# Performance work log

Measured on AMD Instinct MI355X. Metric: run time of the kernel, lower is better.

## Reference

```python
import jax, jax.numpy as jnp
import numpy as np

N = 50000      # nodes
E = 600000     # edges
F_IN = 9       # atom features
H = 128        # hidden dim
G = 2048       # graphs in batch
EPS = 1e-5     # batchnorm eps


def setup_inputs() -> dict:
    key = jax.random.key(0)
    ks = jax.random.split(key, 24)

    def lin(k, i, o):
        return (jax.random.normal(k, (i, o), jnp.float32) / np.sqrt(i).astype(np.float32))

    x = jax.random.normal(ks[0], (N, F_IN), jnp.float32)
    edge_index = jax.random.randint(ks[1], (2, E), 0, N, dtype=jnp.int32)
    # deterministic sorted graph assignment: every graph non-empty (~24 nodes each)
    batch = ((jnp.arange(N, dtype=jnp.int32) * G) // N).astype(jnp.int32)

    return {
        "x": x, "edge_index": edge_index, "batch": batch,
        "W0": lin(ks[2], F_IN, H), "b0": jnp.zeros((H,), jnp.float32),
        "g0": jnp.ones((H,), jnp.float32), "be0": jnp.zeros((H,), jnp.float32),
        "W1": lin(ks[3], H, H), "b1": jnp.zeros((H,), jnp.float32),
        "g1": jnp.ones((H,), jnp.float32), "be1": jnp.zeros((H,), jnp.float32),
        "W2": lin(ks[4], H, H), "b2": jnp.zeros((H,), jnp.float32),
        "g2": jnp.ones((H,), jnp.float32), "be2": jnp.zeros((H,), jnp.float32),
        "fc1_w": lin(ks[5], 2 * H, H), "fc1_b": jnp.zeros((H,), jnp.float32),
        "fc2_w": lin(ks[6], H, H // 2), "fc2_b": jnp.zeros((H // 2,), jnp.float32),
        "out_w": lin(ks[7], H // 2, 5), "out_b": jnp.zeros((5,), jnp.float32),
    }


def _gcn_conv(x, src, dst, W, b):
    # PyG GCNConv: add self-loops, symmetric deg^-1/2 normalization.
    h = x @ W                                   # [N, H_out]
    deg = jax.ops.segment_sum(jnp.ones((E,), h.dtype), dst, num_segments=N) + 1.0
    dis = jax.lax.rsqrt(deg)                    # deg^-1/2 incl. self-loop
    coef = dis[src] * dis[dst]                  # [E]
    agg = jax.ops.segment_sum(h[src] * coef[:, None], dst, num_segments=N)
    agg = agg + h * (dis * dis)[:, None]        # self-loop messages
    return agg + b


def _bn_relu(x, g, b):
    m = jnp.mean(x, axis=0)
    v = jnp.mean(jnp.square(x - m), axis=0)     # biased variance (torch BN)
    return jax.nn.relu((x - m) * jax.lax.rsqrt(v + EPS) * g + b)


def reference(x, edge_index, batch,
              W0, b0, g0, be0, W1, b1, g1, be1, W2, b2, g2, be2,
              fc1_w, fc1_b, fc2_w, fc2_b, out_w, out_b):
    src, dst = edge_index[0], edge_index[1]

    h = _bn_relu(_gcn_conv(x, src, dst, W0, b0), g0, be0)
    h = _bn_relu(_gcn_conv(h, src, dst, W1, b1), g1, be1)
    h = _bn_relu(_gcn_conv(h, src, dst, W2, b2), g2, be2)

    counts = jax.ops.segment_sum(jnp.ones((N,), h.dtype), batch, num_segments=G)
    x_mean = jax.ops.segment_sum(h, batch, num_segments=G) / jnp.maximum(counts, 1.0)[:, None]
    x_max = jax.ops.segment_max(h, batch, num_segments=G)

    z = jnp.concatenate([x_mean, x_max], axis=1)        # [G, 2H]
    z = jax.nn.relu(z @ fc1_w + fc1_b)
    z = jax.nn.relu(z @ fc2_w + fc2_b)
    return z @ out_w + out_b                            # [G, 5]
```

## Files before the change

kernel.cpp:

```cpp
#include <hip/hip_runtime.h>
#include <hip/hip_bf16.h>

#define N_NODES 50000
#define N_EDGES 600000
#define F_INX 9
#define HD 128
#define G_GRAPHS 2048
#define BN_EPS 1e-5f

#define SCAN_CHUNK 1024
#define SCAN_BLOCKS ((N_NODES + SCAN_CHUNK - 1) / SCAN_CHUNK)
#define BN_SLICES 16
#define BN_LAYER_F (BN_SLICES * 256)

#define NB_LIN0 3125
#define NB_WCONV 16
#define NB_ZCNT 196
#define NB_ZBN 48
#define NB_PRE (NB_LIN0 + NB_WCONV + NB_ZCNT + NB_ZBN)

typedef __bf16 bf16x8 __attribute__((ext_vector_type(8)));
typedef float f32x4 __attribute__((ext_vector_type(4)));

__device__ inline unsigned short f2bf(float f) {
    union { float f; unsigned u; } v;
    v.f = f;
    unsigned r = v.u + 0x7fff + ((v.u >> 16) & 1);
    return (unsigned short)(r >> 16);
}
__device__ inline float asf(unsigned u) {
    union { unsigned u; float f; } v;
    v.u = u;
    return v.f;
}
__device__ inline unsigned packbf(float a, float b) {
    return (unsigned)f2bf(a) | ((unsigned)f2bf(b) << 16);
}

__global__ __launch_bounds__(256) void k_preamble(
        const float* __restrict__ x, const float* __restrict__ W0,
        const float* __restrict__ W1, const float* __restrict__ W2,
        int* __restrict__ cnt, float* __restrict__ bnacc,
        unsigned short* __restrict__ wf1, unsigned short* __restrict__ wf2,
        unsigned short* __restrict__ hout) {
    int b = blockIdx.x, t = threadIdx.x;
    if (b < NB_LIN0) {
        __shared__ float rows[16][F_INX];
        int node0 = b * 16;
        for (int i = t; i < 16 * F_INX; i += 256)
            rows[i / F_INX][i % F_INX] = x[(size_t)node0 * F_INX + i];
        __syncthreads();
        int half = t >> 7, c = t & 127;
        float acc[8];
#pragma unroll
        for (int n = 0; n < 8; ++n) acc[n] = 0.0f;
#pragma unroll
        for (int k = 0; k < F_INX; ++k) {
            float w = W0[k * HD + c];
#pragma unroll
            for (int n = 0; n < 8; ++n) acc[n] += rows[half * 8 + n][k] * w;
        }
#pragma unroll
        for (int n = 0; n < 8; ++n)
            hout[(size_t)(node0 + half * 8 + n) * HD + c] = f2bf(acc[n]);
    } else if (b < NB_LIN0 + NB_WCONV) {
        int bw = b - NB_LIN0;
        const float* W = (bw < 8) ? W1 : W2;
        unsigned short* Wf = (bw < 8) ? wf1 : wf2;
        int triple = (bw & 7) * 256 + t;
        int kb = triple >> 9;
        int rest = triple & 511;
        int nt = rest >> 6;
        int l = rest & 63;
        int quad = l >> 4, lc = l & 15;
#pragma unroll
        for (int j = 0; j < 8; ++j)
            Wf[(size_t)triple * 8 + j] =
                f2bf(W[(size_t)(kb * 32 + quad * 8 + j) * HD + nt * 16 + lc]);
    } else if (b < NB_LIN0 + NB_WCONV + NB_ZCNT) {
        int idx = (b - NB_LIN0 - NB_WCONV) * 256 + t;
        if (idx < N_NODES) cnt[idx] = 0;
    } else {
        int idx = (b - NB_LIN0 - NB_WCONV - NB_ZCNT) * 256 + t;
        if (idx < 3 * BN_LAYER_F) bnacc[idx] = 0.0f;
    }
}

__global__ void k_count(const int* __restrict__ dst, int* __restrict__ cnt) {
    int e = blockIdx.x * blockDim.x + threadIdx.x;
    if (e < N_EDGES) atomicAdd(&cnt[dst[e]], 1);
}

__global__ void k_scanA(const int* __restrict__ cnt, int* __restrict__ blocksum) {
    __shared__ int red[256];
    int b = blockIdx.x, t = threadIdx.x;
    int idx = b * SCAN_CHUNK + t * 4;
    int s = 0;
    if (idx + 3 < N_NODES) {
        int4 v = *(const int4*)(cnt + idx);
        s = v.x + v.y + v.z + v.w;
    }
    red[t] = s;
    __syncthreads();
    for (int off = 128; off > 0; off >>= 1) {
        if (t < off) red[t] += red[t + off];
        __syncthreads();
    }
    if (t == 0) blocksum[b] = red[0];
}

__global__ void k_scanC(const int* __restrict__ cnt, const int* __restrict__ blocksum,
                        int* __restrict__ rowptr, int* __restrict__ cursor,
                        float* __restrict__ dis) {
    __shared__ int pre[256];
    __shared__ int myoff_s;
    int b = blockIdx.x, t = threadIdx.x;
    if (t < 64) {
        int v = (t < SCAN_BLOCKS) ? blocksum[t] : 0;
        int incl = v;
        for (int off = 1; off < 64; off <<= 1) {
            int u = __shfl_up(incl, off, 64);
            if (t >= off) incl += u;
        }
        if (t == b) myoff_s = incl - v;
    }
    int idx = b * SCAN_CHUNK + t * 4;
    int4 v = make_int4(0, 0, 0, 0);
    bool valid = (idx + 3 < N_NODES);
    if (valid) v = *(const int4*)(cnt + idx);
    int s = v.x + v.y + v.z + v.w;
    pre[t] = s;
    __syncthreads();
    for (int off = 1; off < 256; off <<= 1) {
        int u = (t >= off) ? pre[t - off] : 0;
        __syncthreads();
        pre[t] += u;
        __syncthreads();
    }
    if (valid) {
        int base = myoff_s + pre[t] - s;
        int4 rp;
        rp.x = base;
        rp.y = base + v.x;
        rp.z = rp.y + v.y;
        rp.w = rp.z + v.z;
        *(int4*)(rowptr + idx) = rp;
        *(int4*)(cursor + idx) = rp;
        float4 dv = make_float4(rsqrtf((float)v.x + 1.0f), rsqrtf((float)v.y + 1.0f),
                                rsqrtf((float)v.z + 1.0f), rsqrtf((float)v.w + 1.0f));
        *(float4*)(dis + idx) = dv;
    }
}

__global__ void k_scatter(const int* __restrict__ src, const int* __restrict__ dst,
                          const float* __restrict__ dis, int* __restrict__ cursor,
                          unsigned* __restrict__ ebuf) {
    int e = blockIdx.x * blockDim.x + threadIdx.x;
    if (e >= N_EDGES) return;
    int s = src[e], d = dst[e];
    int pos = atomicAdd(&cursor[d], 1);
    float coef = dis[s] * dis[d];
    ebuf[pos] = (unsigned)(s & 0xffff) | ((unsigned)f2bf(coef) << 16);
}

#define LIN_ROWS 64
#define ATS 136

__global__ __launch_bounds__(256, 4) void k_linear_mfma(
        const unsigned* __restrict__ agg32, const unsigned short* __restrict__ Wf,
        const float* __restrict__ bnp, const float* __restrict__ gam,
        const float* __restrict__ bet, unsigned short* __restrict__ hout) {
    __shared__ __align__(16) unsigned short At[LIN_ROWS][ATS];
    __shared__ float sc_s[HD], sh_s[HD];
    int node0 = blockIdx.x * LIN_ROWS;
    int t = threadIdx.x;

    if (t < HD) {
        float s = 0.0f, q = 0.0f;
#pragma unroll
        for (int i = 0; i < BN_SLICES; ++i) {
            s += bnp[i * 256 + t];
            q += bnp[i * 256 + 128 + t];
        }
        const float inv_n = 1.0f / (float)N_NODES;
        float m = s * inv_n;
        float v = q * inv_n - m * m;
        float sc = gam[t] * rsqrtf(v + BN_EPS);
        sc_s[t] = sc;
        sh_s[t] = bet[t] - m * sc;
    }
    __syncthreads();

    for (int i = t; i < LIN_ROWS * 16; i += 256) {
        int r = i >> 4;
        int c8 = (i & 15) * 8;
        int node = node0 + r;
        uint4 u = make_uint4(0, 0, 0, 0);
        if (node < N_NODES) u = *(const uint4*)(agg32 + (size_t)node * 64 + c8 / 2);
        unsigned uu[4] = {u.x, u.y, u.z, u.w};
        unsigned short o[8];
#pragma unroll
        for (int j = 0; j < 4; ++j) {
            float e = asf(uu[j] << 16);
            float od = asf(uu[j] & 0xffff0000u);
            int ce = c8 + 2 * j, co = ce + 1;
            o[2 * j] = f2bf(fmaxf(0.f, e * sc_s[ce] + sh_s[ce]));
            o[2 * j + 1] = f2bf(fmaxf(0.f, od * sc_s[co] + sh_s[co]));
        }
        *(ushort4*)&At[r][c8] = *(ushort4*)&o[0];
        *(ushort4*)&At[r][c8 + 4] = *(ushort4*)&o[4];
    }
    __syncthreads();

    int w = t >> 6, l = t & 63;
    int quad = l >> 4, lc = l & 15;
    int arow = w * 16 + lc;
    int koff = quad * 8;

    f32x4 acc[8];
#pragma unroll
    for (int nt = 0; nt < 8; ++nt) acc[nt] = (f32x4){0.f, 0.f, 0.f, 0.f};

#pragma unroll
    for (int kb = 0; kb < 4; ++kb) {
        bf16x8 af = *(const bf16x8*)&At[arow][kb * 32 + koff];
#pragma unroll
        for (int nt = 0; nt < 8; ++nt) {
            bf16x8 bfg = *(const bf16x8*)&Wf[(size_t)(((kb * 8) + nt) * 64 + l) * 8];
            acc[nt] = __builtin_amdgcn_mfma_f32_16x16x32_bf16(af, bfg, acc[nt], 0, 0, 0);
        }
    }

    int node_base = node0 + w * 16 + quad * 4;
#pragma unroll
    for (int nt = 0; nt < 8; ++nt) {
#pragma unroll
        for (int r = 0; r < 4; ++r) {
            int node = node_base + r;
            if (node < N_NODES)
                hout[(size_t)node * HD + nt * 16 + lc] = f2bf(acc[nt][r]);
        }
    }
}

__global__ __launch_bounds__(256, 8) void k_gather(
        const int* __restrict__ rowptr, const int* __restrict__ cnt,
        const unsigned* __restrict__ ebuf, const unsigned short* __restrict__ h,
        const float* __restrict__ dis, unsigned* __restrict__ agg32,
        float* __restrict__ bnp) {
    __shared__ float redS[4][256];
    __shared__ float redQ[4][256];
    int wv = threadIdx.x >> 6;
    int lane = threadIdx.x & 63;
    int node = __builtin_amdgcn_readfirstlane(blockIdx.x * 4 + wv);
    const unsigned* h32 = (const unsigned*)h;

    int start = rowptr[node];
    int deg = cnt[node];
    float d = dis[node];
    unsigned sv = h32[(size_t)node * 64 + lane];
    float dd = d * d;
    float acc0 = asf(sv << 16) * dd;
    float acc1 = asf(sv & 0xffff0000u) * dd;

    int e = start, end = start + deg;
    for (; e + 4 <= end; e += 4) {
        unsigned r0 = ebuf[e], r1 = ebuf[e + 1], r2 = ebuf[e + 2], r3 = ebuf[e + 3];
        unsigned hv0 = h32[(size_t)(r0 & 0xffffu) * 64 + lane];
        unsigned hv1 = h32[(size_t)(r1 & 0xffffu) * 64 + lane];
        unsigned hv2 = h32[(size_t)(r2 & 0xffffu) * 64 + lane];
        unsigned hv3 = h32[(size_t)(r3 & 0xffffu) * 64 + lane];
        float c0 = asf(r0 & 0xffff0000u), c1 = asf(r1 & 0xffff0000u);
        float c2 = asf(r2 & 0xffff0000u), c3 = asf(r3 & 0xffff0000u);
        acc0 += asf(hv0 << 16) * c0;
        acc1 += asf(hv0 & 0xffff0000u) * c0;
        acc0 += asf(hv1 << 16) * c1;
        acc1 += asf(hv1 & 0xffff0000u) * c1;
        acc0 += asf(hv2 << 16) * c2;
        acc1 += asf(hv2 & 0xffff0000u) * c2;
        acc0 += asf(hv3 << 16) * c3;
        acc1 += asf(hv3 & 0xffff0000u) * c3;
    }
    for (; e < end; ++e) {
        unsigned r = ebuf[e];
        unsigned hv = h32[(size_t)(r & 0xffffu) * 64 + lane];
        float cf = asf(r & 0xffff0000u);
        acc0 += asf(hv << 16) * cf;
        acc1 += asf(hv & 0xffff0000u) * cf;
    }

    agg32[(size_t)node * 64 + lane] = packbf(acc0, acc1);

    redS[wv][2 * lane] = acc0;
    redS[wv][2 * lane + 1] = acc1;
    redQ[wv][2 * lane] = acc0 * acc0;
    redQ[wv][2 * lane + 1] = acc1 * acc1;
    __syncthreads();
    int t = threadIdx.x;
    int ch = t & 127;
    int which = t >> 7;
    float val;
    if (which == 0)
        val = redS[0][ch] + redS[1][ch] + redS[2][ch] + redS[3][ch];
    else
        val = redQ[0][ch] + redQ[1][ch] + redQ[2][ch] + redQ[3][ch];
    int slice = blockIdx.x & (BN_SLICES - 1);
    atomicAdd(&bnp[slice * 256 + which * 128 + ch], val);
}

__global__ void k_head(const unsigned short* __restrict__ agg16,
                       const float* __restrict__ bnp, const float* __restrict__ gam,
                       const float* __restrict__ bet, const float* __restrict__ fc1_w,
                       const float* __restrict__ fc1_b, const float* __restrict__ fc2_w,
                       const float* __restrict__ fc2_b, const float* __restrict__ out_w,
                       const float* __restrict__ out_b, float* __restrict__ out) {
    __shared__ float z[2 * HD];
    __shared__ float z1[HD];
    __shared__ float z2[64];
    int g = blockIdx.x, c = threadIdx.x;
    float s = 0.0f, q = 0.0f;
#pragma unroll
    for (int i = 0; i < BN_SLICES; ++i) {
        s += bnp[i * 256 + c];
        q += bnp[i * 256 + 128 + c];
    }
    const float inv_n = 1.0f / (float)N_NODES;
    float m = s * inv_n;
    float v = q * inv_n - m * m;
    float sc = gam[c] * rsqrtf(v + BN_EPS);
    float sh = bet[c] - m * sc;
    int start = (g * N_NODES + G_GRAPHS - 1) / G_GRAPHS;
    int end = ((g + 1) * N_NODES + G_GRAPHS - 1) / G_GRAPHS;
    float sm = 0.0f, mx = 0.0f;
    for (int n = start; n < end; ++n) {
        float raw = asf((unsigned)agg16[(size_t)n * HD + c] << 16);
        float val = fmaxf(0.0f, raw * sc + sh);
        sm += val;
        mx = fmaxf(mx, val);
    }
    z[c] = sm / (float)(end - start);
    z[HD + c] = mx;
    __syncthreads();
    float a1 = fc1_b[c];
#pragma unroll 8
    for (int k = 0; k < 2 * HD; ++k) a1 += z[k] * fc1_w[k * HD + c];
    z1[c] = fmaxf(a1, 0.0f);
    __syncthreads();
    if (c < 64) {
        float a2 = fc2_b[c];
#pragma unroll 8
        for (int k = 0; k < HD; ++k) a2 += z1[k] * fc2_w[k * 64 + c];
        z2[c] = fmaxf(a2, 0.0f);
    }
    __syncthreads();
    if (c < 5) {
        float a3 = out_b[c];
#pragma unroll
        for (int k = 0; k < 64; ++k) a3 += z2[k] * out_w[k * 5 + c];
        out[(size_t)g * 5 + c] = a3;
    }
}

extern "C" void kernel_launch(void* const* d_in, const int* in_sizes, int n_in,
                              void* d_out, int out_size, void* d_ws, size_t ws_size,
                              hipStream_t stream) {
    const float* x = (const float*)d_in[0];
    const int* edge_index = (const int*)d_in[1];
    const float* W0 = (const float*)d_in[3];
    const float* g0 = (const float*)d_in[5];
    const float* be0 = (const float*)d_in[6];
    const float* W1 = (const float*)d_in[7];
    const float* g1 = (const float*)d_in[9];
    const float* be1 = (const float*)d_in[10];
    const float* W2 = (const float*)d_in[11];
    const float* g2 = (const float*)d_in[13];
    const float* be2 = (const float*)d_in[14];
    const float* fc1_w = (const float*)d_in[15];
    const float* fc1_b = (const float*)d_in[16];
    const float* fc2_w = (const float*)d_in[17];
    const float* fc2_b = (const float*)d_in[18];
    const float* out_w = (const float*)d_in[19];
    const float* out_b = (const float*)d_in[20];
    float* out = (float*)d_out;

    const int* src = edge_index;
    const int* dst = edge_index + N_EDGES;

    char* ws = (char*)d_ws;
    size_t off = 0;
    auto alloc = [&](size_t bytes) {
        char* p = ws + off;
        off += (bytes + 255) & ~(size_t)255;
        return p;
    };
    int* cnt = (int*)alloc(N_NODES * 4);
    int* rowptr = (int*)alloc(N_NODES * 4);
    int* cursor = (int*)alloc(N_NODES * 4);
    float* dis = (float*)alloc(N_NODES * 4);
    int* blocksum = (int*)alloc(SCAN_BLOCKS * 4);
    unsigned* ebuf = (unsigned*)alloc((size_t)N_EDGES * 4);
    unsigned short* hbuf = (unsigned short*)alloc((size_t)N_NODES * HD * 2);
    unsigned* aggbuf = (unsigned*)alloc((size_t)N_NODES * 64 * 4);
    float* bnacc = (float*)alloc((size_t)3 * BN_LAYER_F * 4);
    unsigned short* wf1 = (unsigned short*)alloc(HD * HD * 2);
    unsigned short* wf2 = (unsigned short*)alloc(HD * HD * 2);
    (void)ws_size;

    float* bnp0 = bnacc + 0 * BN_LAYER_F;
    float* bnp1 = bnacc + 1 * BN_LAYER_F;
    float* bnp2 = bnacc + 2 * BN_LAYER_F;

    k_preamble<<<NB_PRE, 256, 0, stream>>>(x, W0, W1, W2, cnt, bnacc, wf1, wf2, hbuf);
    k_count<<<(N_EDGES + 255) / 256, 256, 0, stream>>>(dst, cnt);
    k_scanA<<<SCAN_BLOCKS, 256, 0, stream>>>(cnt, blocksum);
    k_scanC<<<SCAN_BLOCKS, 256, 0, stream>>>(cnt, blocksum, rowptr, cursor, dis);
    k_scatter<<<(N_EDGES + 255) / 256, 256, 0, stream>>>(src, dst, dis, cursor, ebuf);

    const int LIN_GRID = (N_NODES + LIN_ROWS - 1) / LIN_ROWS;
    const int GATHER_GRID = N_NODES / 4;

    k_gather<<<GATHER_GRID, 256, 0, stream>>>(rowptr, cnt, ebuf, hbuf, dis, aggbuf, bnp0);
    k_linear_mfma<<<LIN_GRID, 256, 0, stream>>>(aggbuf, wf1, bnp0, g0, be0, hbuf);
    k_gather<<<GATHER_GRID, 256, 0, stream>>>(rowptr, cnt, ebuf, hbuf, dis, aggbuf, bnp1);
    k_linear_mfma<<<LIN_GRID, 256, 0, stream>>>(aggbuf, wf2, bnp1, g1, be1, hbuf);
    k_gather<<<GATHER_GRID, 256, 0, stream>>>(rowptr, cnt, ebuf, hbuf, dis, aggbuf, bnp2);

    k_head<<<G_GRAPHS, HD, 0, stream>>>((const unsigned short*)aggbuf, bnp2, g2, be2,
                                        fc1_w, fc1_b, fc2_w, fc2_b, out_w, out_b, out);
}
```

Baseline: 330.4 us.

## Coarsen gather to four nodes per wave with 16-wide batched edge loads

Each wave in the gather kernel now processes four destination nodes in sequence instead of one, and the grid shrinks to match. The edge loop issues 16 predicated edge-record loads and 16 neighbour-row loads before accumulating, so more memory requests are in flight per wave. Per-wave BN partial sums are accumulated across the four nodes, which cuts shared-memory reductions and global atomics by four. The cost is fewer total waves, so load balancing and latency hiding across waves suffer, and padded lanes issue wasted loads of row 0 because average degree is around 12.

```diff
diff --git a/kernel.cpp b/kernel.cpp
--- a/kernel.cpp
+++ b/kernel.cpp
@@ -243,6 +243,8 @@
     }
 }
 
+#define GN 16
+
 __global__ __launch_bounds__(256, 8) void k_gather(
         const int* __restrict__ rowptr, const int* __restrict__ cnt,
         const unsigned* __restrict__ ebuf, const unsigned short* __restrict__ h,
@@ -252,49 +254,50 @@
     __shared__ float redQ[4][256];
     int wv = threadIdx.x >> 6;
     int lane = threadIdx.x & 63;
-    int node = __builtin_amdgcn_readfirstlane(blockIdx.x * 4 + wv);
     const unsigned* h32 = (const unsigned*)h;
-
-    int start = rowptr[node];
-    int deg = cnt[node];
-    float d = dis[node];
-    unsigned sv = h32[(size_t)node * 64 + lane];
-    float dd = d * d;
-    float acc0 = asf(sv << 16) * dd;
-    float acc1 = asf(sv & 0xffff0000u) * dd;
-
-    int e = start, end = start + deg;
-    for (; e + 4 <= end; e += 4) {
-        unsigned r0 = ebuf[e], r1 = ebuf[e + 1], r2 = ebuf[e + 2], r3 = ebuf[e + 3];
-        unsigned hv0 = h32[(size_t)(r0 & 0xffffu) * 64 + lane];
-        unsigned hv1 = h32[(size_t)(r1 & 0xffffu) * 64 + lane];
-        unsigned hv2 = h32[(size_t)(r2 & 0xffffu) * 64 + lane];
-        unsigned hv3 = h32[(size_t)(r3 & 0xffffu) * 64 + lane];
-        float c0 = asf(r0 & 0xffff0000u), c1 = asf(r1 & 0xffff0000u);
-        float c2 = asf(r2 & 0xffff0000u), c3 = asf(r3 & 0xffff0000u);
-        acc0 += asf(hv0 << 16) * c0;
-        acc1 += asf(hv0 & 0xffff0000u) * c0;
-        acc0 += asf(hv1 << 16) * c1;
-        acc1 += asf(hv1 & 0xffff0000u) * c1;
-        acc0 += asf(hv2 << 16) * c2;
-        acc1 += asf(hv2 & 0xffff0000u) * c2;
-        acc0 += asf(hv3 << 16) * c3;
-        acc1 += asf(hv3 & 0xffff0000u) * c3;
-    }
-    for (; e < end; ++e) {
-        unsigned r = ebuf[e];
-        unsigned hv = h32[(size_t)(r & 0xffffu) * 64 + lane];
-        float cf = asf(r & 0xffff0000u);
-        acc0 += asf(hv << 16) * cf;
-        acc1 += asf(hv & 0xffff0000u) * cf;
-    }
-
-    agg32[(size_t)node * 64 + lane] = packbf(acc0, acc1);
-
-    redS[wv][2 * lane] = acc0;
-    redS[wv][2 * lane + 1] = acc1;
-    redQ[wv][2 * lane] = acc0 * acc0;
-    redQ[wv][2 * lane + 1] = acc1 * acc1;
+    int nodebase = blockIdx.x * GN + wv * 4;
+
+    float s0 = 0.f, s1 = 0.f, q0 = 0.f, q1 = 0.f;
+#pragma unroll
+    for (int i = 0; i < 4; ++i) {
+        int node = __builtin_amdgcn_readfirstlane(nodebase + i);
+        int start = rowptr[node];
+        int deg = cnt[node];
+        float d = dis[node];
+        unsigned sv = h32[(size_t)node * 64 + lane];
+        float dd = d * d;
+        float acc0 = asf(sv << 16) * dd;
+        float acc1 = asf(sv & 0xffff0000u) * dd;
+        int end = start + deg;
+        for (int e0 = start; e0 < end; e0 += 16) {
+            unsigned recs[16];
+#pragma unroll
+            for (int j = 0; j < 16; ++j) {
+                int idx = e0 + j;
+                recs[j] = (idx < end) ? ebuf[idx] : 0u;
+            }
+            unsigned hv[16];
+#pragma unroll
+            for (int j = 0; j < 16; ++j)
+                hv[j] = h32[(size_t)(recs[j] & 0xffffu) * 64 + lane];
+#pragma unroll
+            for (int j = 0; j < 16; ++j) {
+                float cf = asf(recs[j] & 0xffff0000u);
+                acc0 += asf(hv[j] << 16) * cf;
+                acc1 += asf(hv[j] & 0xffff0000u) * cf;
+            }
+        }
+        agg32[(size_t)node * 64 + lane] = packbf(acc0, acc1);
+        s0 += acc0;
+        s1 += acc1;
+        q0 += acc0 * acc0;
+        q1 += acc1 * acc1;
+    }
+
+    redS[wv][2 * lane] = s0;
+    redS[wv][2 * lane + 1] = s1;
+    redQ[wv][2 * lane] = q0;
+    redQ[wv][2 * lane + 1] = q1;
     __syncthreads();
     int t = threadIdx.x;
     int ch = t & 127;
@@ -417,7 +420,7 @@
     k_scatter<<<(N_EDGES + 255) / 256, 256, 0, stream>>>(src, dst, dis, cursor, ebuf);
 
     const int LIN_GRID = (N_NODES + LIN_ROWS - 1) / LIN_ROWS;
-    const int GATHER_GRID = N_NODES / 4;
+    const int GATHER_GRID = N_NODES / GN;
 
     k_gather<<<GATHER_GRID, 256, 0, stream>>>(rowptr, cnt, ebuf, hbuf, dis, aggbuf, bnp0);
     k_linear_mfma<<<LIN_GRID, 256, 0, stream>>>(aggbuf, wf1, bnp0, g0, be0, hbuf);
```

New measurement: 299.3 us. -9.4%, faster.
